# Kernel optimization log

Hardware: AMD Instinct MI355X
Metric: run time of the kernel (lower is better)

Reference implementation:

```python
import jax, jax.numpy as jnp
import numpy as np

B, S, D = 8, 4096, 512
Q, C = 8, 1024


def setup_inputs() -> dict:
    key = jax.random.key(0)
    kx, kc = jax.random.split(key)
    x = jax.random.normal(kx, (B, S, D), dtype=jnp.float32)
    # learned codebooks for each residual quantizer level: [Q, C, D]
    codebooks = jax.random.normal(kc, (Q, C, D), dtype=jnp.float32)
    return {"x": x, "codebooks": codebooks}


def reference(x, codebooks):
    """Residual VQ: cascaded nearest-codebook lookups over residuals.

    Returns (quantized_out, indices [B,S,Q], commit_losses [Q]).
    """

    def step(carry, cb):
        residual, quant_out = carry
        # squared-distance argmin; ||r||^2 term is constant over codes, drop it
        # dist[b,s,c] ~ ||cb_c||^2 - 2 <r_bs, cb_c>
        dist = jnp.sum(cb * cb, axis=-1) - 2.0 * jnp.einsum("bsd,cd->bsc", residual, cb)
        idx = jnp.argmin(dist, axis=-1)            # [B, S]
        q = cb[idx]                                 # [B, S, D] gather
        commit = jnp.mean((jax.lax.stop_gradient(q) - residual) ** 2)
        # straight-through estimator
        q_st = residual + jax.lax.stop_gradient(q - residual)
        new_residual = residual - jax.lax.stop_gradient(q)
        return (new_residual, quant_out + q_st), (idx, commit)

    init = (x, jnp.zeros_like(x))
    (_, quantized), (indices, losses) = jax.lax.scan(step, init, codebooks)
    indices = jnp.transpose(indices, (1, 2, 0))  # [B, S, Q]
    return quantized, indices, losses
```

## Files before the change

kernel.cpp:

```cpp
#include <hip/hip_runtime.h>

#define BD 8
#define SD 4096
#define DDIM 512
#define QD 8
#define CDN 1024
#define ROWS (BD * SD)
#define QUANT_ELEMS (ROWS * DDIM)
#define IDX_OFF QUANT_ELEMS
#define LOSS_OFF (QUANT_ELEMS + ROWS * QD)

#define TPB 256
#define NWAVE (TPB / 64)
#define BR 32
#define MARGIN 0.375f

#define WS_LOSS 0
#define WS_FBCNT 64
#define WS_FBLIST 4096
#define WS_NORMS 0x40000
#define WS_PK 0x100000
#define WS_RESID 0x1100000

typedef __attribute__((ext_vector_type(8))) short short8;
typedef __attribute__((ext_vector_type(8))) _Float16 half8;
typedef __attribute__((ext_vector_type(4))) float f32x4;

__global__ __launch_bounds__(256) void vq_norms(const float* __restrict__ cb,
                                                float* __restrict__ norms) {
    int code = blockIdx.x * 4 + (threadIdx.x >> 6);
    int lane = threadIdx.x & 63;
    const float4* p = (const float4*)(cb + (size_t)code * DDIM);
    float4 a = p[lane];
    float4 b = p[lane + 64];
    float s = a.x * a.x + a.y * a.y + a.z * a.z + a.w * a.w +
              b.x * b.x + b.y * b.y + b.z * b.z + b.w * b.w;
#pragma unroll
    for (int m = 32; m >= 1; m >>= 1) s += __shfl_xor(s, m);
    if (lane == 0) norms[code] = s;
}

__global__ __launch_bounds__(256) void vq_cbpack(const float* __restrict__ cbs,
                                                 ushort* __restrict__ pk) {
    int sg = blockIdx.x * 256 + threadIdx.x;
    int lvl = sg >> 16;
    int s = sg & 65535;
    int tile = s >> 10;
    int kc = (s >> 6) & 15;
    int ln = s & 63;
    int code = tile * 16 + (ln & 15);
    int k0 = kc * 32 + (ln >> 4) * 8;
    const float* p = cbs + (size_t)lvl * CDN * DDIM + (size_t)code * DDIM + k0;
    float f[8];
    *(float4*)&f[0] = *(const float4*)p;
    *(float4*)&f[4] = *(const float4*)(p + 4);
    _Float16 h[8];
#pragma unroll
    for (int i = 0; i < 8; i++) h[i] = (_Float16)f[i];
    *(short8*)(pk + (size_t)sg * 8) = *(short8*)h;
}

__global__ __launch_bounds__(TPB, 2) void vq_level_mfma(
    const float* __restrict__ rsrc, const float* __restrict__ qsub,
    float* __restrict__ resid, float* __restrict__ quant,
    const float* __restrict__ cbq, const float* __restrict__ normq,
    const ushort* __restrict__ pk,
    float* __restrict__ idx_out, double* __restrict__ lossq,
    int* __restrict__ fbCnt, int* __restrict__ fbList, int q) {
    __shared__ ushort Ah[BR * 512];
    __shared__ float s_nrm[CDN];
    __shared__ float m_d1[NWAVE][BR], m_d2[NWAVE][BR], m_d3[NWAVE][BR];
    __shared__ int m_i1[NWAVE][BR], m_i2[NWAVE][BR];
    __shared__ int s_i1[BR], s_i2[BR], s_flag[BR];
    __shared__ double s_part[NWAVE];

    int tid = threadIdx.x;
    int lane = tid & 63;
    int l15 = lane & 15;
    int quad = lane >> 4;
    int cg = tid >> 6;
    int row0 = blockIdx.x * BR;

    for (int i = tid; i < CDN; i += TPB) s_nrm[i] = normq[i];

#pragma unroll
    for (int i = 0; i < 8; i++) {
        int flat = tid + TPB * i;
        int row = flat >> 6;
        int c = flat & 63;
        size_t g = (size_t)(row0 + row) * DDIM + c * 8;
        float f[8];
        *(float4*)&f[0] = *(const float4*)(rsrc + g);
        *(float4*)&f[4] = *(const float4*)(rsrc + g + 4);
        if (qsub) {
            float4 w0 = *(const float4*)(qsub + g);
            float4 w1 = *(const float4*)(qsub + g + 4);
            f[0] -= w0.x; f[1] -= w0.y; f[2] -= w0.z; f[3] -= w0.w;
            f[4] -= w1.x; f[5] -= w1.y; f[6] -= w1.z; f[7] -= w1.w;
        }
        _Float16 h[8];
#pragma unroll
        for (int k = 0; k < 8; k++) h[k] = (_Float16)f[k];
        int dst = row * 512 + ((c ^ (row & 7)) * 8);
        *(short8*)(Ah + dst) = *(short8*)h;
    }
    __syncthreads();

    float td1[8], td2[8], td3[8];
    int t12[8];
#pragma unroll
    for (int s = 0; s < 8; s++) { td1[s] = 3.4e38f; td2[s] = 3.4e38f; td3[s] = 3.4e38f; t12[s] = 0; }

    half8 aR[2][2], bR[2][4];
    f32x4 acc[2][4];
    int aswz = l15 & 7;

#define LOADB(g, p) { int ct_ = (g) >> 4, kc_ = (g) & 15; \
    int base_ = ct_ * 131072 + cg * 32768 + kc_ * 512 + lane * 8; \
    _Pragma("unroll") for (int j = 0; j < 4; j++) \
        bR[p][j] = *(const half8*)(pk + base_ + j * 8192); }

#define LOADA(g, p) { int c0_ = (((g) & 15) * 4 + quad) ^ aswz; \
    aR[p][0] = *(half8*)(Ah + l15 * 512 + c0_ * 8); \
    aR[p][1] = *(half8*)(Ah + (16 + l15) * 512 + c0_ * 8); }

#define BODY(g, p) { \
    if (((g) & 15) == 0) { \
        _Pragma("unroll") for (int rt = 0; rt < 2; rt++) \
        _Pragma("unroll") for (int j = 0; j < 4; j++) acc[rt][j] = (f32x4)0.0f; } \
    if ((g) < 63) { LOADB((g) + 1, 1 - (p)); LOADA((g) + 1, 1 - (p)); } \
    _Pragma("unroll") for (int j = 0; j < 4; j++) { \
        acc[0][j] = __builtin_amdgcn_mfma_f32_16x16x32_f16(aR[p][0], bR[p][j], acc[0][j], 0, 0, 0); \
        acc[1][j] = __builtin_amdgcn_mfma_f32_16x16x32_f16(aR[p][1], bR[p][j], acc[1][j], 0, 0, 0); } \
    if (((g) & 15) == 15) { int ct_ = (g) >> 4; \
        _Pragma("unroll") for (int j = 0; j < 4; j++) { \
            int tile = ct_ * 16 + cg * 4 + j; \
            float nrm = s_nrm[tile * 16 + l15]; \
            _Pragma("unroll") for (int rt = 0; rt < 2; rt++) \
            _Pragma("unroll") for (int reg = 0; reg < 4; reg++) { \
                float v = nrm - 2.0f * acc[rt][j][reg]; \
                int s = rt * 4 + reg; \
                bool b1 = v < td1[s]; bool b2 = v < td2[s]; bool b3 = v < td3[s]; \
                int pb1 = ((t12[s] & 63) << 6) | tile; \
                int pb2 = (tile << 6) | (t12[s] & 63); \
                td3[s] = b2 ? td2[s] : (b3 ? v : td3[s]); \
                t12[s] = b1 ? pb1 : (b2 ? pb2 : t12[s]); \
                td2[s] = b1 ? td1[s] : (b2 ? v : td2[s]); \
                td1[s] = b1 ? v : td1[s]; } } } }

    LOADB(0, 0); LOADA(0, 0);
    for (int gp = 0; gp < 32; gp++) {
        int g0 = gp * 2;
        BODY(g0, 0);
        BODY(g0 + 1, 1);
    }
#undef LOADB
#undef LOADA
#undef BODY

    int ti1[8], ti2[8];
#pragma unroll
    for (int s = 0; s < 8; s++) {
        ti1[s] = (t12[s] & 63) * 16 + l15;
        ti2[s] = ((t12[s] >> 6) & 63) * 16 + l15;
    }

#pragma unroll
    for (int m = 1; m <= 8; m <<= 1) {
#pragma unroll
        for (int s = 0; s < 8; s++) {
            float o1 = __shfl_xor(td1[s], m); int oi1 = __shfl_xor(ti1[s], m);
            float o2 = __shfl_xor(td2[s], m); int oi2 = __shfl_xor(ti2[s], m);
            float o3 = __shfl_xor(td3[s], m);
            bool aw = (td1[s] < o1) || (td1[s] == o1 && ti1[s] < oi1);
            float w2 = aw ? td2[s] : o2; int wi2 = aw ? ti2[s] : oi2;
            float w3 = aw ? td3[s] : o3;
            float n1 = aw ? td1[s] : o1; int ni1 = aw ? ti1[s] : oi1;
            float p1 = aw ? o1 : td1[s]; int pi1 = aw ? oi1 : ti1[s];
            float p2 = aw ? o2 : td2[s];
            bool sw = (w2 < p1) || (w2 == p1 && wi2 < pi1);
            float n2 = sw ? w2 : p1; int ni2 = sw ? wi2 : pi1;
            float n3 = sw ? fminf(p1, w3) : fminf(w2, p2);
            td1[s] = n1; ti1[s] = ni1; td2[s] = n2; ti2[s] = ni2; td3[s] = n3;
        }
    }

    if (l15 == 0) {
#pragma unroll
        for (int s = 0; s < 8; s++) {
            int row = (s >> 2) * 16 + quad * 4 + (s & 3);
            m_d1[cg][row] = td1[s]; m_i1[cg][row] = ti1[s];
            m_d2[cg][row] = td2[s]; m_i2[cg][row] = ti2[s];
            m_d3[cg][row] = td3[s];
        }
    }
    __syncthreads();

    if (tid < BR) {
        int r = tid;
        float d1 = m_d1[0][r]; int i1 = m_i1[0][r];
        float d2 = m_d2[0][r]; int i2 = m_i2[0][r];
        float d3 = m_d3[0][r];
#pragma unroll
        for (int c = 1; c < NWAVE; c++) {
            float o1 = m_d1[c][r]; int oi1 = m_i1[c][r];
            float o2 = m_d2[c][r]; int oi2 = m_i2[c][r];
            float o3 = m_d3[c][r];
            bool aw = (d1 < o1) || (d1 == o1 && i1 < oi1);
            float w2 = aw ? d2 : o2; int wi2 = aw ? i2 : oi2;
            float w3 = aw ? d3 : o3;
            float n1 = aw ? d1 : o1; int ni1 = aw ? i1 : oi1;
            float p1 = aw ? o1 : d1; int pi1 = aw ? oi1 : i1;
            float p2 = aw ? o2 : d2;
            bool sw = (w2 < p1) || (w2 == p1 && wi2 < pi1);
            float n2 = sw ? w2 : p1; int ni2 = sw ? wi2 : pi1;
            float n3 = sw ? fminf(p1, w3) : fminf(w2, p2);
            d1 = n1; i1 = ni1; d2 = n2; i2 = ni2; d3 = n3;
        }
        int flag = 0;
        if (d3 - d1 < MARGIN) flag = 2;
        else if (d2 - d1 < MARGIN) flag = 1;
        s_i1[r] = i1; s_i2[r] = i2; s_flag[r] = flag;
        if (flag == 2) {
            int p = atomicAdd(fbCnt, 1);
            if (p < 32768) fbList[p] = row0 + r;
        }
    }
    __syncthreads();

    for (int r = cg; r < BR; r += NWAVE) {
        if (s_flag[r] != 1) continue;
        int i1 = s_i1[r], i2 = s_i2[r];
        size_t g = (size_t)(row0 + r) * DDIM + lane * 8;
        float rv[8];
        *(float4*)&rv[0] = *(const float4*)(rsrc + g);
        *(float4*)&rv[4] = *(const float4*)(rsrc + g + 4);
        if (qsub) {
            float4 w0 = *(const float4*)(qsub + g);
            float4 w1 = *(const float4*)(qsub + g + 4);
            rv[0] -= w0.x; rv[1] -= w0.y; rv[2] -= w0.z; rv[3] -= w0.w;
            rv[4] -= w1.x; rv[5] -= w1.y; rv[6] -= w1.z; rv[7] -= w1.w;
        }
        float c1[8], c2[8];
        *(float4*)&c1[0] = *(const float4*)(cbq + (size_t)i1 * DDIM + lane * 8);
        *(float4*)&c1[4] = *(const float4*)(cbq + (size_t)i1 * DDIM + lane * 8 + 4);
        *(float4*)&c2[0] = *(const float4*)(cbq + (size_t)i2 * DDIM + lane * 8);
        *(float4*)&c2[4] = *(const float4*)(cbq + (size_t)i2 * DDIM + lane * 8 + 4);
        float e1 = 0.0f, e2 = 0.0f;
#pragma unroll
        for (int i = 0; i < 8; i++) { e1 = fmaf(rv[i], c1[i], e1); e2 = fmaf(rv[i], c2[i], e2); }
#pragma unroll
        for (int m = 32; m >= 1; m >>= 1) { e1 += __shfl_xor(e1, m); e2 += __shfl_xor(e2, m); }
        float dd1 = s_nrm[i1] - 2.0f * e1;
        float dd2 = s_nrm[i2] - 2.0f * e2;
        bool take2 = (dd2 < dd1) || (dd2 == dd1 && i2 < i1);
        if (lane == 0) s_i1[r] = take2 ? i2 : i1;
    }
    __syncthreads();

    if (tid < BR) idx_out[(size_t)(row0 + tid) * QD + q] = (float)s_i1[tid];

    double ls = 0.0;
#pragma unroll 4
    for (int it = 0; it < 16; it++) {
        int flat = tid + TPB * it;
        int row = flat >> 7;
        int c4 = (flat & 127) * 4;
        if (s_flag[row] == 2) continue;
        size_t g = (size_t)(row0 + row) * DDIM + c4;
        float4 r = *(const float4*)(rsrc + g);
        if (qsub) {
            float4 w = *(const float4*)(qsub + g);
            r.x -= w.x; r.y -= w.y; r.z -= w.z; r.w -= w.w;
        }
        float4 cv = *(const float4*)(cbq + (size_t)s_i1[row] * DDIM + c4);
        float4 nr;
        nr.x = r.x - cv.x; nr.y = r.y - cv.y; nr.z = r.z - cv.z; nr.w = r.w - cv.w;
        if (resid) {
            *(float4*)(resid + g) = nr;
        } else {
            float4 qo = *(float4*)(quant + g);
            qo.x += cv.x; qo.y += cv.y; qo.z += cv.z; qo.w += cv.w;
            *(float4*)(quant + g) = qo;
        }
        ls += (double)nr.x * nr.x + (double)nr.y * nr.y +
              (double)nr.z * nr.z + (double)nr.w * nr.w;
    }
#pragma unroll
    for (int m = 32; m >= 1; m >>= 1) ls += __shfl_down(ls, m);
    if ((tid & 63) == 0) s_part[tid >> 6] = ls;
    __syncthreads();
    if (tid == 0) {
        double t = s_part[0] + s_part[1] + s_part[2] + s_part[3];
        atomicAdd(lossq, t);
    }
}

__global__ __launch_bounds__(256) void vq_fallback(
    const float* __restrict__ rsrc, const float* __restrict__ qsub,
    float* __restrict__ resid, float* __restrict__ quant,
    const float* __restrict__ cbq, const float* __restrict__ normq,
    float* __restrict__ idx_out, double* __restrict__ lossq,
    const int* __restrict__ fbCnt, const int* __restrict__ fbList, int q) {
    __shared__ float r_s[DDIM];
    __shared__ unsigned long long s_best;
    int tid = threadIdx.x;
    int n = *fbCnt; if (n > 32768) n = 32768;
    for (int w = blockIdx.x; w < n; w += gridDim.x) {
        int row = fbList[w];
        if (tid == 0) s_best = ~0ull;
        if (tid < 128) {
            size_t g = (size_t)row * DDIM + tid * 4;
            float4 v = *(const float4*)(rsrc + g);
            if (qsub) {
                float4 x = *(const float4*)(qsub + g);
                v.x -= x.x; v.y -= x.y; v.z -= x.z; v.w -= x.w;
            }
            *(float4*)&r_s[tid * 4] = v;
        }
        __syncthreads();
#pragma unroll
        for (int cc = 0; cc < 4; cc++) {
            int c = tid + 256 * cc;
            float dot = 0.0f;
            for (int k4 = 0; k4 < 128; k4++) {
                float4 cv = *(const float4*)(cbq + (size_t)c * DDIM + k4 * 4);
                float4 rv = *(const float4*)&r_s[k4 * 4];
                dot = fmaf(cv.x, rv.x, dot); dot = fmaf(cv.y, rv.y, dot);
                dot = fmaf(cv.z, rv.z, dot); dot = fmaf(cv.w, rv.w, dot);
            }
            float dist = normq[c] - 2.0f * dot;
            unsigned b = __float_as_uint(dist);
            b = (b & 0x80000000u) ? ~b : (b | 0x80000000u);
            unsigned long long key = (((unsigned long long)b) << 32) | (unsigned)c;
            atomicMin(&s_best, key);
        }
        __syncthreads();
        int idx = (int)(s_best & 0xffffffffull);
        if (tid == 0) idx_out[(size_t)row * QD + q] = (float)idx;
        double ls = 0.0;
        if (tid < 128) {
            size_t g = (size_t)row * DDIM + tid * 4;
            float4 r = *(const float4*)&r_s[tid * 4];
            float4 cv = *(const float4*)(cbq + (size_t)idx * DDIM + tid * 4);
            float4 nr;
            nr.x = r.x - cv.x; nr.y = r.y - cv.y; nr.z = r.z - cv.z; nr.w = r.w - cv.w;
            if (resid) {
                *(float4*)(resid + g) = nr;
            } else {
                float4 qo = *(float4*)(quant + g);
                qo.x += cv.x; qo.y += cv.y; qo.z += cv.z; qo.w += cv.w;
                *(float4*)(quant + g) = qo;
            }
            ls = (double)nr.x * nr.x + (double)nr.y * nr.y +
                 (double)nr.z * nr.z + (double)nr.w * nr.w;
        }
#pragma unroll
        for (int m = 32; m >= 1; m >>= 1) ls += __shfl_down(ls, m);
        if ((tid & 63) == 0 && ls != 0.0) atomicAdd(lossq, ls);
        __syncthreads();
    }
}

__global__ __launch_bounds__(256) void vq_quant_final(const float* __restrict__ x,
                                                      const float* __restrict__ resid,
                                                      float* __restrict__ quant) {
    size_t i = ((size_t)blockIdx.x * 256 + threadIdx.x) * 4;
    float4 xv = *(const float4*)(x + i);
    float4 rv = *(const float4*)(resid + i);
    float4 o;
    o.x = xv.x - rv.x; o.y = xv.y - rv.y; o.z = xv.z - rv.z; o.w = xv.w - rv.w;
    *(float4*)(quant + i) = o;
}

__global__ void vq_loss_final(const double* __restrict__ lossws, float* __restrict__ out) {
    int i = threadIdx.x;
    if (i < QD) out[i] = (float)(lossws[i] * (1.0 / (double)((size_t)ROWS * DDIM)));
}

extern "C" void kernel_launch(void* const* d_in, const int* in_sizes, int n_in,
                              void* d_out, int out_size, void* d_ws, size_t ws_size,
                              hipStream_t stream) {
    const float* x = (const float*)d_in[0];
    const float* cbs = (const float*)d_in[1];
    float* out = (float*)d_out;
    float* quant = out;
    float* idxo = out + IDX_OFF;
    float* losso = out + LOSS_OFF;

    char* ws = (char*)d_ws;
    double* lossws = (double*)(ws + WS_LOSS);
    int* fbCnt = (int*)(ws + WS_FBCNT);
    int* fbList = (int*)(ws + WS_FBLIST);
    float* norms = (float*)(ws + WS_NORMS);
    ushort* pk = (ushort*)(ws + WS_PK);
    float* resid = (ws_size >= (size_t)WS_RESID + (size_t)QUANT_ELEMS * 4)
                       ? (float*)(ws + WS_RESID) : nullptr;

    hipMemsetAsync(d_ws, 0, 128, stream);
    if (!resid) hipMemsetAsync(d_out, 0, (size_t)out_size * 4, stream);

    vq_norms<<<QD * CDN / 4, 256, 0, stream>>>(cbs, norms);
    vq_cbpack<<<QD * 256, 256, 0, stream>>>(cbs, pk);

    for (int q = 0; q < QD; q++) {
        const float* cbq = cbs + (size_t)q * CDN * DDIM;
        const float* nq = norms + (size_t)q * CDN;
        const ushort* pq = pk + (size_t)q * CDN * DDIM;
        const float* rsrc;
        const float* qsubA;
        if (resid) {
            rsrc = (q == 0) ? x : resid;
            qsubA = nullptr;
        } else {
            rsrc = x;
            qsubA = quant;
        }
        vq_level_mfma<<<ROWS / BR, TPB, 0, stream>>>(
            rsrc, qsubA, resid, quant, cbq, nq, pq,
            idxo, lossws + q, fbCnt + q, fbList, q);
        vq_fallback<<<256, 256, 0, stream>>>(
            rsrc, qsubA, resid, quant, cbq, nq, idxo, lossws + q,
            fbCnt + q, fbList, q);
    }
    if (resid) {
        vq_quant_final<<<QUANT_ELEMS / 1024, 256, 0, stream>>>(x, resid, quant);
    }
    vq_loss_final<<<1, 64, 0, stream>>>(lossws, losso);
}
```

Baseline: 1.494 ms.

## Fuse exact fallback search and final quant write into level kernel

Rows whose top candidates fall within the margin now get an exact FP32 full-codebook search inside the level kernel, which stages the residual in reused shared memory, instead of going through a global list and a separate fallback kernel. The last level writes quantized = x - residual directly, so the separate final elementwise kernel is gone. Together these cut eight fallback launches, the atomic list and a full-tensor pass. The cost is that a block with ambiguous rows now stalls serially on the exact search, which can unbalance the level kernel.

After: 1.511 ms. About the same (+1.1%).

```diff
diff --git a/kernel.cpp b/kernel.cpp
--- a/kernel.cpp
+++ b/kernel.cpp
@@ -16,8 +16,6 @@
 #define MARGIN 0.375f
 
 #define WS_LOSS 0
-#define WS_FBCNT 64
-#define WS_FBLIST 4096
 #define WS_NORMS 0x40000
 #define WS_PK 0x100000
 #define WS_RESID 0x1100000
@@ -63,16 +61,17 @@
 __global__ __launch_bounds__(TPB, 2) void vq_level_mfma(
     const float* __restrict__ rsrc, const float* __restrict__ qsub,
     float* __restrict__ resid, float* __restrict__ quant,
+    const float* __restrict__ xfin,
     const float* __restrict__ cbq, const float* __restrict__ normq,
     const ushort* __restrict__ pk,
-    float* __restrict__ idx_out, double* __restrict__ lossq,
-    int* __restrict__ fbCnt, int* __restrict__ fbList, int q) {
+    float* __restrict__ idx_out, double* __restrict__ lossq, int q) {
     __shared__ ushort Ah[BR * 512];
     __shared__ float s_nrm[CDN];
     __shared__ float m_d1[NWAVE][BR], m_d2[NWAVE][BR], m_d3[NWAVE][BR];
     __shared__ int m_i1[NWAVE][BR], m_i2[NWAVE][BR];
     __shared__ int s_i1[BR], s_i2[BR], s_flag[BR];
     __shared__ double s_part[NWAVE];
+    __shared__ unsigned long long s_best;
 
     int tid = threadIdx.x;
     int lane = tid & 63;
@@ -221,10 +220,6 @@
         if (d3 - d1 < MARGIN) flag = 2;
         else if (d2 - d1 < MARGIN) flag = 1;
         s_i1[r] = i1; s_i2[r] = i2; s_flag[r] = flag;
-        if (flag == 2) {
-            int p = atomicAdd(fbCnt, 1);
-            if (p < 32768) fbList[p] = row0 + r;
-        }
     }
     __syncthreads();
 
@@ -258,63 +253,16 @@
     }
     __syncthreads();
 
-    if (tid < BR) idx_out[(size_t)(row0 + tid) * QD + q] = (float)s_i1[tid];
-
-    double ls = 0.0;
-#pragma unroll 4
-    for (int it = 0; it < 16; it++) {
-        int flat = tid + TPB * it;
-        int row = flat >> 7;
-        int c4 = (flat & 127) * 4;
-        if (s_flag[row] == 2) continue;
-        size_t g = (size_t)(row0 + row) * DDIM + c4;
-        float4 r = *(const float4*)(rsrc + g);
-        if (qsub) {
-            float4 w = *(const float4*)(qsub + g);
-            r.x -= w.x; r.y -= w.y; r.z -= w.z; r.w -= w.w;
-        }
-        float4 cv = *(const float4*)(cbq + (size_t)s_i1[row] * DDIM + c4);
-        float4 nr;
-        nr.x = r.x - cv.x; nr.y = r.y - cv.y; nr.z = r.z - cv.z; nr.w = r.w - cv.w;
-        if (resid) {
-            *(float4*)(resid + g) = nr;
-        } else {
-            float4 qo = *(float4*)(quant + g);
-            qo.x += cv.x; qo.y += cv.y; qo.z += cv.z; qo.w += cv.w;
-            *(float4*)(quant + g) = qo;
-        }
-        ls += (double)nr.x * nr.x + (double)nr.y * nr.y +
-              (double)nr.z * nr.z + (double)nr.w * nr.w;
-    }
-#pragma unroll
-    for (int m = 32; m >= 1; m >>= 1) ls += __shfl_down(ls, m);
-    if ((tid & 63) == 0) s_part[tid >> 6] = ls;
-    __syncthreads();
-    if (tid == 0) {
-        double t = s_part[0] + s_part[1] + s_part[2] + s_part[3];
-        atomicAdd(lossq, t);
-    }
-}
-
-__global__ __launch_bounds__(256) void vq_fallback(
-    const float* __restrict__ rsrc, const float* __restrict__ qsub,
-    float* __restrict__ resid, float* __restrict__ quant,
-    const float* __restrict__ cbq, const float* __restrict__ normq,
-    float* __restrict__ idx_out, double* __restrict__ lossq,
-    const int* __restrict__ fbCnt, const int* __restrict__ fbList, int q) {
-    __shared__ float r_s[DDIM];
-    __shared__ unsigned long long s_best;
-    int tid = threadIdx.x;
-    int n = *fbCnt; if (n > 32768) n = 32768;
-    for (int w = blockIdx.x; w < n; w += gridDim.x) {
-        int row = fbList[w];
+    float* r_s = (float*)Ah;
+    for (int r = 0; r < BR; r++) {
+        if (s_flag[r] != 2) continue;
         if (tid == 0) s_best = ~0ull;
         if (tid < 128) {
-            size_t g = (size_t)row * DDIM + tid * 4;
+            size_t g = (size_t)(row0 + r) * DDIM + tid * 4;
             float4 v = *(const float4*)(rsrc + g);
             if (qsub) {
-                float4 x = *(const float4*)(qsub + g);
-                v.x -= x.x; v.y -= x.y; v.z -= x.z; v.w -= x.w;
+                float4 xx = *(const float4*)(qsub + g);
+                v.x -= xx.x; v.y -= xx.y; v.z -= xx.z; v.w -= xx.w;
             }
             *(float4*)&r_s[tid * 4] = v;
         }
@@ -329,48 +277,57 @@
                 dot = fmaf(cv.x, rv.x, dot); dot = fmaf(cv.y, rv.y, dot);
                 dot = fmaf(cv.z, rv.z, dot); dot = fmaf(cv.w, rv.w, dot);
             }
-            float dist = normq[c] - 2.0f * dot;
+            float dist = s_nrm[c] - 2.0f * dot;
             unsigned b = __float_as_uint(dist);
             b = (b & 0x80000000u) ? ~b : (b | 0x80000000u);
             unsigned long long key = (((unsigned long long)b) << 32) | (unsigned)c;
             atomicMin(&s_best, key);
         }
         __syncthreads();
-        int idx = (int)(s_best & 0xffffffffull);
-        if (tid == 0) idx_out[(size_t)row * QD + q] = (float)idx;
-        double ls = 0.0;
-        if (tid < 128) {
-            size_t g = (size_t)row * DDIM + tid * 4;
-            float4 r = *(const float4*)&r_s[tid * 4];
-            float4 cv = *(const float4*)(cbq + (size_t)idx * DDIM + tid * 4);
-            float4 nr;
-            nr.x = r.x - cv.x; nr.y = r.y - cv.y; nr.z = r.z - cv.z; nr.w = r.w - cv.w;
-            if (resid) {
-                *(float4*)(resid + g) = nr;
-            } else {
-                float4 qo = *(float4*)(quant + g);
-                qo.x += cv.x; qo.y += cv.y; qo.z += cv.z; qo.w += cv.w;
-                *(float4*)(quant + g) = qo;
-            }
-            ls = (double)nr.x * nr.x + (double)nr.y * nr.y +
-                 (double)nr.z * nr.z + (double)nr.w * nr.w;
-        }
-#pragma unroll
-        for (int m = 32; m >= 1; m >>= 1) ls += __shfl_down(ls, m);
-        if ((tid & 63) == 0 && ls != 0.0) atomicAdd(lossq, ls);
+        if (tid == 0) s_i1[r] = (int)(s_best & 0xffffffffull);
         __syncthreads();
     }
-}
-
-__global__ __launch_bounds__(256) void vq_quant_final(const float* __restrict__ x,
-                                                      const float* __restrict__ resid,
-                                                      float* __restrict__ quant) {
-    size_t i = ((size_t)blockIdx.x * 256 + threadIdx.x) * 4;
-    float4 xv = *(const float4*)(x + i);
-    float4 rv = *(const float4*)(resid + i);
-    float4 o;
-    o.x = xv.x - rv.x; o.y = xv.y - rv.y; o.z = xv.z - rv.z; o.w = xv.w - rv.w;
-    *(float4*)(quant + i) = o;
+
+    if (tid < BR) idx_out[(size_t)(row0 + tid) * QD + q] = (float)s_i1[tid];
+
+    double ls = 0.0;
+#pragma unroll 4
+    for (int it = 0; it < 16; it++) {
+        int flat = tid + TPB * it;
+        int row = flat >> 7;
+        int c4 = (flat & 127) * 4;
+        size_t g = (size_t)(row0 + row) * DDIM + c4;
+        float4 r = *(const float4*)(rsrc + g);
+        if (qsub) {
+            float4 w = *(const float4*)(qsub + g);
+            r.x -= w.x; r.y -= w.y; r.z -= w.z; r.w -= w.w;
+        }
+        float4 cv = *(const float4*)(cbq + (size_t)s_i1[row] * DDIM + c4);
+        float4 nr;
+        nr.x = r.x - cv.x; nr.y = r.y - cv.y; nr.z = r.z - cv.z; nr.w = r.w - cv.w;
+        if (xfin) {
+            float4 xv = *(const float4*)(xfin + g);
+            float4 qo;
+            qo.x = xv.x - nr.x; qo.y = xv.y - nr.y; qo.z = xv.z - nr.z; qo.w = xv.w - nr.w;
+            *(float4*)(quant + g) = qo;
+        } else if (resid) {
+            *(float4*)(resid + g) = nr;
+        } else {
+            float4 qo = *(float4*)(quant + g);
+            qo.x += cv.x; qo.y += cv.y; qo.z += cv.z; qo.w += cv.w;
+            *(float4*)(quant + g) = qo;
+        }
+        ls += (double)nr.x * nr.x + (double)nr.y * nr.y +
+              (double)nr.z * nr.z + (double)nr.w * nr.w;
+    }
+#pragma unroll
+    for (int m = 32; m >= 1; m >>= 1) ls += __shfl_down(ls, m);
+    if ((tid & 63) == 0) s_part[tid >> 6] = ls;
+    __syncthreads();
+    if (tid == 0) {
+        double t = s_part[0] + s_part[1] + s_part[2] + s_part[3];
+        atomicAdd(lossq, t);
+    }
 }
 
 __global__ void vq_loss_final(const double* __restrict__ lossws, float* __restrict__ out) {
@@ -390,14 +347,12 @@
 
     char* ws = (char*)d_ws;
     double* lossws = (double*)(ws + WS_LOSS);
-    int* fbCnt = (int*)(ws + WS_FBCNT);
-    int* fbList = (int*)(ws + WS_FBLIST);
     float* norms = (float*)(ws + WS_NORMS);
     ushort* pk = (ushort*)(ws + WS_PK);
     float* resid = (ws_size >= (size_t)WS_RESID + (size_t)QUANT_ELEMS * 4)
                        ? (float*)(ws + WS_RESID) : nullptr;
 
-    hipMemsetAsync(d_ws, 0, 128, stream);
+    hipMemsetAsync(d_ws, 0, 64, stream);
     if (!resid) hipMemsetAsync(d_out, 0, (size_t)out_size * 4, stream);
 
     vq_norms<<<QD * CDN / 4, 256, 0, stream>>>(cbs, norms);
@@ -409,22 +364,18 @@
         const ushort* pq = pk + (size_t)q * CDN * DDIM;
         const float* rsrc;
         const float* qsubA;
+        const float* xfin = nullptr;
         if (resid) {
             rsrc = (q == 0) ? x : resid;
             qsubA = nullptr;
+            if (q == QD - 1) xfin = x;
         } else {
             rsrc = x;
             qsubA = quant;
         }
         vq_level_mfma<<<ROWS / BR, TPB, 0, stream>>>(
-            rsrc, qsubA, resid, quant, cbq, nq, pq,
-            idxo, lossws + q, fbCnt + q, fbList, q);
-        vq_fallback<<<256, 256, 0, stream>>>(
-            rsrc, qsubA, resid, quant, cbq, nq, idxo, lossws + q,
-            fbCnt + q, fbList, q);
-    }
-    if (resid) {
-        vq_quant_final<<<QUANT_ELEMS / 1024, 256, 0, stream>>>(x, resid, quant);
+            rsrc, qsubA, resid, quant, xfin, cbq, nq, pq,
+            idxo, lossws + q, q);
     }
     vq_loss_final<<<1, 64, 0, stream>>>(lossws, losso);
 }
```
